# Kernel tuning notes

Hardware: AMD Instinct MI355X
Metric: run time of the kernel (lower is better)

## Reference

```python
import jax, jax.numpy as jnp
import numpy as np

B, T, M, P = 512, 64, 256, 256


def setup_inputs() -> dict:
    key = jax.random.key(0)
    ks = jax.random.split(key, 17)
    w = lambda i, shape: (jax.random.normal(ks[i], shape, jnp.float32) * 0.05)
    return {
        "encoded_inputs": jax.random.normal(ks[0], (B, T, M), jnp.float32),
        "y": jax.random.normal(ks[1], (B, T, 1), jnp.float32),
        "tar": jax.random.normal(ks[2], (B, 2), jnp.float32),
        "train": 1,
        "Wd_w": w(3, (M, 2 * P)), "Wd_b": w(4, (M,)),
        "Ud_w": w(5, (M, M)),
        "vd_w": w(6, (1, M)),
        "wt_w": w(7, (1, M + 1)), "wt_b": w(8, (1,)),
        "Wy_w": w(9, (P, P + M)), "Wy_b": w(10, (P,)),
        "vy_w": w(11, (1, P)), "vy_b": w(12, (1,)),
        "Wih": w(13, (4 * P, 1)), "Whh": w(14, (4 * P, P)),
        "bih": w(15, (4 * P,)), "bhh": w(16, (4 * P,)),
    }


def _lstm_cell(x, h, c, Wih, Whh, bih, bhh):
    # torch.nn.LSTMCell gate order: i, f, g, o
    g = x @ Wih.T + h @ Whh.T + (bih + bhh)
    i, f, gg, o = jnp.split(g, 4, axis=1)
    c = jax.nn.sigmoid(f) * c + jax.nn.sigmoid(i) * jnp.tanh(gg)
    h = jax.nn.sigmoid(o) * jnp.tanh(c)
    return h, c


def reference(encoded_inputs, y, tar, train,
              Wd_w, Wd_b, Ud_w, vd_w, wt_w, wt_b,
              Wy_w, Wy_b, vy_w, vy_b, Wih, Whh, bih, bhh):
    Bn = encoded_inputs.shape[0]
    Pn = Whh.shape[1]
    Mn = encoded_inputs.shape[2]
    h0 = jnp.zeros((Bn, Pn), encoded_inputs.dtype)
    c0 = jnp.zeros((Bn, Pn), encoded_inputs.dtype)
    ctx0 = jnp.zeros((Bn, Mn), encoded_inputs.dtype)
    # U_d(encoded_inputs) is loop-invariant
    y1 = jnp.einsum('btm,nm->btn', encoded_inputs, Ud_w)  # (B,T,M)

    def attend(h, s):
        x1 = jnp.concatenate([h, s], axis=1) @ Wd_w.T + Wd_b      # (B,M)
        z1 = jnp.tanh(x1[:, None, :] + y1)                        # (B,T,M)
        l = jnp.einsum('btm,m->bt', z1, vd_w[0])                  # (B,T)
        beta = jax.nn.softmax(l, axis=1)
        return jnp.einsum('bt,btm->bm', beta, encoded_inputs)     # (B,M)

    def step(carry, y_t):
        h, s, _ = carry
        c_t = attend(h, s)
        y_til = jnp.concatenate([c_t, y_t], axis=1) @ wt_w.T + wt_b  # (B,1)
        h, s = _lstm_cell(y_til, h, s, Wih, Whh, bih, bhh)
        return (h, s, c_t), None

    (h, s, c_t), _ = jax.lax.scan(step, (h0, c0, ctx0), jnp.swapaxes(y, 0, 1))

    def head(h):
        return (jnp.concatenate([h, c_t], axis=1) @ Wy_w.T + Wy_b) @ vy_w.T + vy_b

    def extra(h, s, inp):
        y_til = jnp.concatenate([c_t, inp], axis=1) @ wt_w.T + wt_b
        h, s = _lstm_cell(y_til, h, s, Wih, Whh, bih, bhh)
        return h, s, head(h)

    y_Tp1 = head(h)
    if train:
        h, s, y_Tp2 = extra(h, s, tar[:, 0:1])
        h, s, y_Tp3 = extra(h, s, tar[:, 1:2])
    else:
        h, s, y_Tp2 = extra(h, s, y_Tp1)
        h, s, y_Tp3 = extra(h, s, y_Tp2)
    return (y_Tp1, y_Tp2, y_Tp3)
```

## Files before the change

kernel.cpp:

```cpp
#include <hip/hip_runtime.h>


typedef unsigned short u16;
typedef unsigned int u32;
typedef _Float16 half_t;
typedef half_t h2 __attribute__((ext_vector_type(2)));

#define BB 512
#define TT 64
#define MM 256
#define PP 256
#define YS 264
#define ES 68

#define WD16_OFF  0
#define WHH16_OFF 131072
#define WY16_OFF  393216
#define WQ_ELEMS  524288
#define WQ_BYTES  (WQ_ELEMS * 2)

struct H8 { h2 p[4]; };

#if defined(__has_builtin)
#if __has_builtin(__builtin_amdgcn_fdot2)
#define FDOT2(a, b, c) __builtin_amdgcn_fdot2((a), (b), (c), false)
#endif
#endif
#ifndef FDOT2
__device__ __forceinline__ float FDOT2(h2 a, h2 b, float c) {
  return c + (float)a[0] * (float)b[0] + (float)a[1] * (float)b[1];
}
#endif

__device__ __forceinline__ float dot8(const H8 w, const H8 a, float acc) {
  acc = FDOT2(w.p[0], a.p[0], acc);
  acc = FDOT2(w.p[1], a.p[1], acc);
  acc = FDOT2(w.p[2], a.p[2], acc);
  acc = FDOT2(w.p[3], a.p[3], acc);
  return acc;
}
__device__ __forceinline__ u16 f2h(float f) {
  union { half_t h; u16 u; } x; x.h = (half_t)f; return x.u;
}
__device__ __forceinline__ void unpackH8(const H8 v, float f[8]) {
#pragma unroll
  for (int i = 0; i < 8; ++i) f[i] = (float)v.p[i >> 1][i & 1];
}
__device__ __forceinline__ void ldf8(const float* p, float f[8]) {
  float4 a = *(const float4*)p;
  float4 b = *(const float4*)(p + 4);
  f[0]=a.x; f[1]=a.y; f[2]=a.z; f[3]=a.w;
  f[4]=b.x; f[5]=b.y; f[6]=b.z; f[7]=b.w;
}
__device__ __forceinline__ float tanh_fast(float x) {
  float e = __builtin_amdgcn_exp2f(x * 2.885390081777927f);
  return 1.0f - 2.0f * __builtin_amdgcn_rcpf(1.0f + e);
}
__device__ __forceinline__ float sigmoid_fast(float x) {
  float e = __builtin_amdgcn_exp2f(x * -1.4426950408889634f);
  return __builtin_amdgcn_rcpf(1.0f + e);
}

__global__ __launch_bounds__(256) void prep_kernel(
    const float* __restrict__ Wd, const float* __restrict__ Whh,
    const float* __restrict__ Wy, u16* __restrict__ o) {
  int i = blockIdx.x * 256 + threadIdx.x;
  float v;
  if (i < WHH16_OFF) {
    int ki = i & 7, n = (i >> 3) & 255, kb = i >> 11;
    v = Wd[n * 512 + kb * 8 + ki];
  } else if (i < WY16_OFF) {
    int r = i - WHH16_OFF;
    int ki = r & 7, n = (r >> 3) & 1023, kb = r >> 13;
    v = Whh[n * 256 + kb * 8 + ki];
  } else {
    int r = i - WY16_OFF;
    int ki = r & 7, n = (r >> 3) & 255, kb = r >> 11;
    v = Wy[n * 512 + kb * 8 + ki];
  }
  o[i] = f2h(v);
}

template <int WQ>
__global__ __launch_bounds__(256, 2) void scan_kernel(
    const float* __restrict__ E,
    const float* __restrict__ yin,
    const float* __restrict__ tar,
    const int*   __restrict__ train,
    const void*  __restrict__ Wd_q,
    const float* __restrict__ Wd_b,
    const float* __restrict__ Ud_w,
    const float* __restrict__ vd_w,
    const float* __restrict__ wt_w,
    const float* __restrict__ wt_b,
    const void*  __restrict__ Wy_q,
    const float* __restrict__ Wy_b,
    const float* __restrict__ vy_w,
    const float* __restrict__ vy_b,
    const float* __restrict__ Wih,
    const void*  __restrict__ Whh_q,
    const float* __restrict__ bih,
    const float* __restrict__ bhh,
    float* __restrict__ out)
{
  __shared__ __align__(16) u16   y1l[TT * YS];
  __shared__ __align__(16) u16   e16T[MM * ES];
  __shared__ __align__(16) u32   hs16[256];
  __shared__ __align__(16) u32   ctx16p[128];
  __shared__ __align__(16) float ctx[MM];
  __shared__ __align__(16) float x1s[MM];
  __shared__ __align__(16) float lpart[4][TT];
  __shared__ __align__(16) u16   betas16[TT];
  __shared__ float red[4];
  __shared__ float sc[2];

  const int j = threadIdx.x;
  const int b = blockIdx.x;
  const int wv = j >> 6;

  hs16[j] = 0;
  float creg = 0.f;

  {
    const float* __restrict__ Eb = E + (size_t)b * TT * MM;
    for (int i = j; i < TT * MM; i += 256) {
      int t = i >> 8, m = i & 255;
      e16T[m * ES + t] = f2h(Eb[i]);
    }
  }

  {
    const float* __restrict__ Eb = E + (size_t)b * TT * MM;
    const float* __restrict__ Uj = Ud_w + (size_t)j * MM;
    for (int t0 = 0; t0 < TT; t0 += 16) {
      float acc[16];
#pragma unroll
      for (int i = 0; i < 16; ++i) acc[i] = 0.f;
      for (int m0 = 0; m0 < MM; m0 += 8) {
        float w[8]; ldf8(Uj + m0, w);
#pragma unroll
        for (int tt = 0; tt < 16; ++tt) {
          float e[8]; ldf8(Eb + (size_t)(t0 + tt) * MM + m0, e);
#pragma unroll
          for (int mm = 0; mm < 8; ++mm) acc[tt] = fmaf(e[mm], w[mm], acc[tt]);
        }
      }
#pragma unroll
      for (int tt = 0; tt < 16; ++tt)
        y1l[(t0 + tt) * YS + j] = f2h(acc[tt]);
    }
  }
  __syncthreads();

  auto mv4 = [&](float& g0, float& g1, float& g2, float& g3) {
    g0 = g1 = g2 = g3 = 0.f;
    if (WQ) {
      const u16* W = (const u16*)Whh_q;
      const u16* p0 = W + (size_t)j * 8;
      const u16* p1 = p0 + 256 * 8;
      const u16* p2 = p0 + 512 * 8;
      const u16* p3 = p0 + 768 * 8;
#pragma unroll 4
      for (int kb = 0; kb < 32; ++kb) {
        H8 hp = *(const H8*)&hs16[kb * 4];
        g0 = dot8(*(const H8*)p0, hp, g0); p0 += 8192;
        g1 = dot8(*(const H8*)p1, hp, g1); p1 += 8192;
        g2 = dot8(*(const H8*)p2, hp, g2); p2 += 8192;
        g3 = dot8(*(const H8*)p3, hp, g3); p3 += 8192;
      }
    } else {
      const float* W = (const float*)Whh_q;
      const float* p0 = W + (size_t)j * 256;
#pragma unroll 2
      for (int kb = 0; kb < 32; ++kb) {
        H8 hp = *(const H8*)&hs16[kb * 4];
        float hf[8]; unpackH8(hp, hf);
        float w0[8], w1[8], w2[8], w3[8];
        ldf8(p0 + kb * 8, w0);
        ldf8(p0 + 256 * 256 + kb * 8, w1);
        ldf8(p0 + 512 * 256 + kb * 8, w2);
        ldf8(p0 + 768 * 256 + kb * 8, w3);
#pragma unroll
        for (int i = 0; i < 8; ++i) {
          g0 = fmaf(hf[i], w0[i], g0);
          g1 = fmaf(hf[i], w1[i], g1);
          g2 = fmaf(hf[i], w2[i], g2);
          g3 = fmaf(hf[i], w3[i], g3);
        }
      }
    }
  };

  auto gates_apply = [&](float g0, float g1, float g2, float g3, float ytil) {
    g0 += ytil * Wih[j]       + bih[j]       + bhh[j];
    g1 += ytil * Wih[j + 256] + bih[j + 256] + bhh[j + 256];
    g2 += ytil * Wih[j + 512] + bih[j + 512] + bhh[j + 512];
    g3 += ytil * Wih[j + 768] + bih[j + 768] + bhh[j + 768];
    float c = sigmoid_fast(g1) * creg + sigmoid_fast(g0) * tanh_fast(g2);
    float h = sigmoid_fast(g3) * tanh_fast(c);
    creg = c;
    u16* hsu = (u16*)hs16;
    hsu[j] = f2h(h);
    hsu[256 + j] = f2h(c);
  };

  auto head_store = [&](int outIdx) {
    float p = 0.f;
    if (WQ) {
      const u16* W = (const u16*)Wy_q;
      const u16* ph = W + (size_t)j * 8;
      const u16* pc = W + (size_t)(32 * 256 + j) * 8;
#pragma unroll 4
      for (int kb = 0; kb < 32; ++kb) {
        H8 hp = *(const H8*)&hs16[kb * 4];
        H8 cp = *(const H8*)&ctx16p[kb * 4];
        p = dot8(*(const H8*)ph, hp, p); ph += 2048;
        p = dot8(*(const H8*)pc, cp, p); pc += 2048;
      }
    } else {
      const float* W = (const float*)Wy_q + (size_t)j * 512;
      for (int kb = 0; kb < 32; ++kb) {
        H8 hp = *(const H8*)&hs16[kb * 4];
        float hf[8]; unpackH8(hp, hf);
        float w0[8], w1[8];
        ldf8(W + kb * 8, w0);
        ldf8(W + 256 + kb * 8, w1);
#pragma unroll
        for (int i = 0; i < 8; ++i) {
          p = fmaf(hf[i], w0[i], p);
          p = fmaf(ctx[kb * 8 + i], w1[i], p);
        }
      }
    }
    float pp = (p + Wy_b[j]) * vy_w[j];
#pragma unroll
    for (int off = 32; off; off >>= 1) pp += __shfl_xor(pp, off, 64);
    if ((j & 63) == 0) red[wv] = pp;
    __syncthreads();
    if (j == 0) {
      float o = red[0] + red[1] + red[2] + red[3] + vy_b[0];
      out[(size_t)outIdx * BB + b] = o;
      sc[0] = o;
    }
    __syncthreads();
  };

  for (int step = 0; step < TT; ++step) {
    float ax0 = 0.f, ax1 = 0.f, g0, g1, g2, g3;
    {
      if (WQ) {
        const u16* Wd16 = (const u16*)Wd_q;
        const u16* Wh16 = (const u16*)Whh_q;
        const u16* pdh = Wd16 + (size_t)j * 8;
        const u16* pdc = Wd16 + (size_t)(32 * 256 + j) * 8;
        const u16* p0 = Wh16 + (size_t)j * 8;
        const u16* p1 = p0 + 256 * 8;
        const u16* p2 = p0 + 512 * 8;
        const u16* p3 = p0 + 768 * 8;
        float b0 = 0.f, b1 = 0.f, b2 = 0.f, b3 = 0.f;
#pragma unroll 4
        for (int kb = 0; kb < 32; ++kb) {
          H8 hp = *(const H8*)&hs16[kb * 4];
          H8 cp = *(const H8*)&hs16[128 + kb * 4];
          ax0 = dot8(*(const H8*)pdh, hp, ax0); pdh += 2048;
          ax1 = dot8(*(const H8*)pdc, cp, ax1); pdc += 2048;
          b0 = dot8(*(const H8*)p0, hp, b0); p0 += 8192;
          b1 = dot8(*(const H8*)p1, hp, b1); p1 += 8192;
          b2 = dot8(*(const H8*)p2, hp, b2); p2 += 8192;
          b3 = dot8(*(const H8*)p3, hp, b3); p3 += 8192;
        }
        g0 = b0; g1 = b1; g2 = b2; g3 = b3;
      } else {
        const float* wd = (const float*)Wd_q + (size_t)j * 512;
        const float* w0p = (const float*)Whh_q + (size_t)j * 256;
        float b0 = 0.f, b1 = 0.f, b2 = 0.f, b3 = 0.f;
#pragma unroll 2
        for (int kb = 0; kb < 32; ++kb) {
          H8 hp = *(const H8*)&hs16[kb * 4];
          H8 cp = *(const H8*)&hs16[128 + kb * 4];
          float hf[8], cf[8]; unpackH8(hp, hf); unpackH8(cp, cf);
          float wh[8], wc[8], w0[8], w1[8], w2[8], w3[8];
          ldf8(wd + kb * 8, wh);
          ldf8(wd + 256 + kb * 8, wc);
          ldf8(w0p + kb * 8, w0);
          ldf8(w0p + 256 * 256 + kb * 8, w1);
          ldf8(w0p + 512 * 256 + kb * 8, w2);
          ldf8(w0p + 768 * 256 + kb * 8, w3);
#pragma unroll
          for (int i = 0; i < 8; ++i) {
            ax0 = fmaf(hf[i], wh[i], ax0);
            ax1 = fmaf(cf[i], wc[i], ax1);
            b0 = fmaf(hf[i], w0[i], b0);
            b1 = fmaf(hf[i], w1[i], b1);
            b2 = fmaf(hf[i], w2[i], b2);
            b3 = fmaf(hf[i], w3[i], b3);
          }
        }
        g0 = b0; g1 = b1; g2 = b2; g3 = b3;
      }
      x1s[j] = ax0 + ax1 + Wd_b[j];
    }
    __syncthreads();

    {
      const int q = wv, tq = j & 63;
      const u16* __restrict__ yrow = &y1l[tq * YS + q * 64];
      const float* __restrict__ xp = &x1s[q * 64];
      const float* __restrict__ vp = vd_w + q * 64;
      float lp = 0.f;
#pragma unroll 2
      for (int m0 = 0; m0 < 64; m0 += 8) {
        H8 yv = *(const H8*)(yrow + m0);
        float yf[8]; unpackH8(yv, yf);
        float xf[8]; ldf8(xp + m0, xf);
        float vf[8]; ldf8(vp + m0, vf);
#pragma unroll
        for (int mm = 0; mm < 8; ++mm) {
          float z = tanh_fast(xf[mm] + yf[mm]);
          lp = fmaf(z, vf[mm], lp);
        }
      }
      lpart[q][tq] = lp;
    }
    __syncthreads();

    if (j < 64) {
      const int t = j;
      float l = lpart[0][t] + lpart[1][t] + lpart[2][t] + lpart[3][t];
      float mx = l;
#pragma unroll
      for (int off = 32; off; off >>= 1) mx = fmaxf(mx, __shfl_xor(mx, off, 64));
      float e = __builtin_amdgcn_exp2f((l - mx) * 1.4426950408889634f);
      float sm = e;
#pragma unroll
      for (int off = 32; off; off >>= 1) sm += __shfl_xor(sm, off, 64);
      betas16[t] = f2h(e * __builtin_amdgcn_rcpf(sm));
    }
    __syncthreads();

    {
      const u16* __restrict__ ep = &e16T[j * ES];
      float acc = 0.f;
#pragma unroll
      for (int t0 = 0; t0 < TT; t0 += 8) {
        h2 e0 = *(const h2*)(ep + t0);
        h2 e1 = *(const h2*)(ep + t0 + 2);
        h2 e2 = *(const h2*)(ep + t0 + 4);
        h2 e3 = *(const h2*)(ep + t0 + 6);
        H8 bp = *(const H8*)&betas16[t0];
        acc = FDOT2(bp.p[0], e0, acc);
        acc = FDOT2(bp.p[1], e1, acc);
        acc = FDOT2(bp.p[2], e2, acc);
        acc = FDOT2(bp.p[3], e3, acc);
      }
      ctx[j] = acc;
      ((u16*)ctx16p)[j] = f2h(acc);
    }
    {
      float p = ctx[j] * wt_w[j];
#pragma unroll
      for (int off = 32; off; off >>= 1) p += __shfl_xor(p, off, 64);
      if ((j & 63) == 0) red[wv] = p;
    }
    __syncthreads();
    {
      float ytil = red[0] + red[1] + red[2] + red[3]
                 + yin[(size_t)b * TT + step] * wt_w[MM] + wt_b[0];
      gates_apply(g0, g1, g2, g3, ytil);
    }
    __syncthreads();
  }

  float ctdot;
  {
    float p = ctx[j] * wt_w[j];
#pragma unroll
    for (int off = 32; off; off >>= 1) p += __shfl_xor(p, off, 64);
    if ((j & 63) == 0) red[wv] = p;
    __syncthreads();
    ctdot = red[0] + red[1] + red[2] + red[3];
    __syncthreads();
  }

  head_store(0);

  const int tr = train[0];
  for (int e = 0; e < 2; ++e) {
    float inp = tr ? tar[(size_t)b * 2 + e] : sc[0];
    float ytil = ctdot + inp * wt_w[MM] + wt_b[0];
    float g0, g1, g2, g3;
    mv4(g0, g1, g2, g3);
    gates_apply(g0, g1, g2, g3, ytil);
    __syncthreads();
    head_store(1 + e);
  }
}

extern "C" void kernel_launch(void* const* d_in, const int* in_sizes, int n_in,
                              void* d_out, int out_size, void* d_ws, size_t ws_size,
                              hipStream_t stream) {
  const float* E     = (const float*)d_in[0];
  const float* yin   = (const float*)d_in[1];
  const float* tar   = (const float*)d_in[2];
  const int*   train = (const int*)d_in[3];
  const float* Wd_w  = (const float*)d_in[4];
  const float* Wd_b  = (const float*)d_in[5];
  const float* Ud_w  = (const float*)d_in[6];
  const float* vd_w  = (const float*)d_in[7];
  const float* wt_w  = (const float*)d_in[8];
  const float* wt_b  = (const float*)d_in[9];
  const float* Wy_w  = (const float*)d_in[10];
  const float* Wy_b  = (const float*)d_in[11];
  const float* vy_w  = (const float*)d_in[12];
  const float* vy_b  = (const float*)d_in[13];
  const float* Wih   = (const float*)d_in[14];
  const float* Whh   = (const float*)d_in[15];
  const float* bih   = (const float*)d_in[16];
  const float* bhh   = (const float*)d_in[17];

  float* out = (float*)d_out;

  if (ws_size >= (size_t)WQ_BYTES) {
    u16* wq = (u16*)d_ws;
    prep_kernel<<<dim3(WQ_ELEMS / 256), dim3(256), 0, stream>>>(
        Wd_w, Whh, Wy_w, wq);
    scan_kernel<1><<<dim3(BB), dim3(256), 0, stream>>>(
        E, yin, tar, train, wq + WD16_OFF, Wd_b, Ud_w, vd_w, wt_w, wt_b,
        wq + WY16_OFF, Wy_b, vy_w, vy_b, Wih, wq + WHH16_OFF, bih, bhh, out);
  } else {
    scan_kernel<0><<<dim3(BB), dim3(256), 0, stream>>>(
        E, yin, tar, train, Wd_w, Wd_b, Ud_w, vd_w, wt_w, wt_b,
        Wy_w, Wy_b, vy_w, vy_b, Wih, Whh, bih, bhh, out);
  }

  (void)in_sizes; (void)n_in; (void)out_size;
}
```

Baseline: 1.192 ms.

## Fold context dot into precomputed E·wt and split work over 512 threads

Precomputes E·wt per timestep so the per-step context's wt projection reduces to a softmax-weighted sum of scalars, removing the per-step context vector computation and the fp16 transposed E copy in LDS. Context is only materialised once after the loop for the head. Block size doubles to 512 threads, with the Wd and Wy matvecs split across halves and Whh gates written through shared memory, and loop-invariant LSTM biases hoisted into registers. This trades lower occupancy and extra LDS traffic and syncs for less redundant per-step work.

```diff
diff --git a/kernel.cpp b/kernel.cpp
--- a/kernel.cpp
+++ b/kernel.cpp
@@ -9,9 +9,8 @@
 #define BB 512
 #define TT 64
 #define MM 256
-#define PP 256
 #define YS 264
-#define ES 68
+#define NTH 512
 
 #define WD16_OFF  0
 #define WHH16_OFF 131072
@@ -82,7 +81,7 @@
 }
 
 template <int WQ>
-__global__ __launch_bounds__(256, 2) void scan_kernel(
+__global__ __launch_bounds__(NTH) void scan_kernel(
     const float* __restrict__ E,
     const float* __restrict__ yin,
     const float* __restrict__ tar,
@@ -104,35 +103,52 @@
     float* __restrict__ out)
 {
   __shared__ __align__(16) u16   y1l[TT * YS];
-  __shared__ __align__(16) u16   e16T[MM * ES];
   __shared__ __align__(16) u32   hs16[256];
   __shared__ __align__(16) u32   ctx16p[128];
-  __shared__ __align__(16) float ctx[MM];
-  __shared__ __align__(16) float x1s[MM];
-  __shared__ __align__(16) float lpart[4][TT];
-  __shared__ __align__(16) u16   betas16[TT];
-  __shared__ float red[4];
-  __shared__ float sc[2];
-
-  const int j = threadIdx.x;
-  const int b = blockIdx.x;
-  const int wv = j >> 6;
-
-  hs16[j] = 0;
+  __shared__ __align__(16) float px1[2][MM];
+  __shared__ __align__(16) float gg[1024];
+  __shared__ __align__(16) float lpart[8][TT];
+  __shared__ __align__(16) float bet[TT];
+  __shared__ __align__(16) float ysh[TT];
+  __shared__ __align__(16) float ewl[TT];
+  __shared__ float red[8];
+  __shared__ float sc[1];
+
+  const int j    = threadIdx.x;
+  const int n    = j & 255;
+  const int half = j >> 8;
+  const int wv   = j >> 6;
+  const int b    = blockIdx.x;
+
+  if (j < 256) hs16[j] = 0;
   float creg = 0.f;
+
+  const float wih0 = Wih[n],       wih1 = Wih[n + 256];
+  const float wih2 = Wih[n + 512], wih3 = Wih[n + 768];
+  const float bb0 = bih[n]       + bhh[n];
+  const float bb1 = bih[n + 256] + bhh[n + 256];
+  const float bb2 = bih[n + 512] + bhh[n + 512];
+  const float bb3 = bih[n + 768] + bhh[n + 768];
+  const float wtM = wt_w[MM], wtb = wt_b[0];
+
+  if (j < TT) {
+    const int t = j;
+    ysh[t] = yin[(size_t)b * TT + t];
+    const float* __restrict__ Er = E + ((size_t)b * TT + t) * MM;
+    float acc = 0.f;
+    for (int m0 = 0; m0 < MM; m0 += 8) {
+      float e[8], w[8];
+      ldf8(Er + m0, e); ldf8(wt_w + m0, w);
+#pragma unroll
+      for (int m = 0; m < 8; ++m) acc = fmaf(e[m], w[m], acc);
+    }
+    ewl[t] = acc;
+  }
 
   {
     const float* __restrict__ Eb = E + (size_t)b * TT * MM;
-    for (int i = j; i < TT * MM; i += 256) {
-      int t = i >> 8, m = i & 255;
-      e16T[m * ES + t] = f2h(Eb[i]);
-    }
-  }
-
-  {
-    const float* __restrict__ Eb = E + (size_t)b * TT * MM;
-    const float* __restrict__ Uj = Ud_w + (size_t)j * MM;
-    for (int t0 = 0; t0 < TT; t0 += 16) {
+    const float* __restrict__ Uj = Ud_w + (size_t)n * MM;
+    for (int t0 = half * 32; t0 < half * 32 + 32; t0 += 16) {
       float acc[16];
 #pragma unroll
       for (int i = 0; i < 16; ++i) acc[i] = 0.f;
@@ -147,95 +163,92 @@
       }
 #pragma unroll
       for (int tt = 0; tt < 16; ++tt)
-        y1l[(t0 + tt) * YS + j] = f2h(acc[tt]);
+        y1l[(t0 + tt) * YS + n] = f2h(acc[tt]);
     }
   }
   __syncthreads();
 
-  auto mv4 = [&](float& g0, float& g1, float& g2, float& g3) {
-    g0 = g1 = g2 = g3 = 0.f;
+  auto gates_apply = [&](float gi, float gf, float gG, float go, float ytil) {
+    gi += ytil * wih0 + bb0;
+    gf += ytil * wih1 + bb1;
+    gG += ytil * wih2 + bb2;
+    go += ytil * wih3 + bb3;
+    float c = sigmoid_fast(gf) * creg + sigmoid_fast(gi) * tanh_fast(gG);
+    float h = sigmoid_fast(go) * tanh_fast(c);
+    creg = c;
+    u16* hsu = (u16*)hs16;
+    hsu[n] = f2h(h);
+    hsu[256 + n] = f2h(c);
+  };
+
+  auto whh_gg = [&]() {
+    float g1 = 0.f, g2 = 0.f;
     if (WQ) {
-      const u16* W = (const u16*)Whh_q;
-      const u16* p0 = W + (size_t)j * 8;
-      const u16* p1 = p0 + 256 * 8;
-      const u16* p2 = p0 + 512 * 8;
-      const u16* p3 = p0 + 768 * 8;
+      const u16* __restrict__ pw = (const u16*)Whh_q + (size_t)j * 8;
 #pragma unroll 4
       for (int kb = 0; kb < 32; ++kb) {
-        H8 hp = *(const H8*)&hs16[kb * 4];
-        g0 = dot8(*(const H8*)p0, hp, g0); p0 += 8192;
-        g1 = dot8(*(const H8*)p1, hp, g1); p1 += 8192;
-        g2 = dot8(*(const H8*)p2, hp, g2); p2 += 8192;
-        g3 = dot8(*(const H8*)p3, hp, g3); p3 += 8192;
+        H8 w1 = *(const H8*)pw;
+        H8 w2 = *(const H8*)(pw + 4096);
+        pw += 8192;
+        H8 hv = *(const H8*)&hs16[kb * 4];
+        g1 = dot8(w1, hv, g1);
+        g2 = dot8(w2, hv, g2);
       }
     } else {
-      const float* W = (const float*)Whh_q;
-      const float* p0 = W + (size_t)j * 256;
+      const float* __restrict__ p1 = (const float*)Whh_q + (size_t)j * 256;
+      const float* __restrict__ p2 = (const float*)Whh_q +
+                                     ((size_t)j + 512) * 256;
 #pragma unroll 2
       for (int kb = 0; kb < 32; ++kb) {
-        H8 hp = *(const H8*)&hs16[kb * 4];
-        float hf[8]; unpackH8(hp, hf);
-        float w0[8], w1[8], w2[8], w3[8];
-        ldf8(p0 + kb * 8, w0);
-        ldf8(p0 + 256 * 256 + kb * 8, w1);
-        ldf8(p0 + 512 * 256 + kb * 8, w2);
-        ldf8(p0 + 768 * 256 + kb * 8, w3);
-#pragma unroll
-        for (int i = 0; i < 8; ++i) {
-          g0 = fmaf(hf[i], w0[i], g0);
-          g1 = fmaf(hf[i], w1[i], g1);
-          g2 = fmaf(hf[i], w2[i], g2);
-          g3 = fmaf(hf[i], w3[i], g3);
+        H8 hv = *(const H8*)&hs16[kb * 4];
+        float hf[8]; unpackH8(hv, hf);
+        float w1[8], w2[8];
+        ldf8(p1 + kb * 8, w1); ldf8(p2 + kb * 8, w2);
+#pragma unroll
+        for (int m = 0; m < 8; ++m) {
+          g1 = fmaf(hf[m], w1[m], g1);
+          g2 = fmaf(hf[m], w2[m], g2);
         }
       }
     }
+    gg[j] = g1;
+    gg[j + 512] = g2;
   };
 
-  auto gates_apply = [&](float g0, float g1, float g2, float g3, float ytil) {
-    g0 += ytil * Wih[j]       + bih[j]       + bhh[j];
-    g1 += ytil * Wih[j + 256] + bih[j + 256] + bhh[j + 256];
-    g2 += ytil * Wih[j + 512] + bih[j + 512] + bhh[j + 512];
-    g3 += ytil * Wih[j + 768] + bih[j + 768] + bhh[j + 768];
-    float c = sigmoid_fast(g1) * creg + sigmoid_fast(g0) * tanh_fast(g2);
-    float h = sigmoid_fast(g3) * tanh_fast(c);
-    creg = c;
-    u16* hsu = (u16*)hs16;
-    hsu[j] = f2h(h);
-    hsu[256 + j] = f2h(c);
+  auto gates_from_gg = [&](float ytil) {
+    gates_apply(gg[n], gg[n + 256], gg[n + 512], gg[n + 768], ytil);
   };
 
   auto head_store = [&](int outIdx) {
     float p = 0.f;
+    const u32* st = half ? ctx16p : hs16;
     if (WQ) {
-      const u16* W = (const u16*)Wy_q;
-      const u16* ph = W + (size_t)j * 8;
-      const u16* pc = W + (size_t)(32 * 256 + j) * 8;
-#pragma unroll 4
+      const u16* pw = (const u16*)Wy_q + ((size_t)(half * 32) * 256 + n) * 8;
+#pragma unroll 2
       for (int kb = 0; kb < 32; ++kb) {
-        H8 hp = *(const H8*)&hs16[kb * 4];
-        H8 cp = *(const H8*)&ctx16p[kb * 4];
-        p = dot8(*(const H8*)ph, hp, p); ph += 2048;
-        p = dot8(*(const H8*)pc, cp, p); pc += 2048;
+        H8 w = *(const H8*)pw; pw += 2048;
+        H8 s = *(const H8*)&st[kb * 4];
+        p = dot8(w, s, p);
       }
     } else {
-      const float* W = (const float*)Wy_q + (size_t)j * 512;
+      const float* W = (const float*)Wy_q + (size_t)n * 512 + half * 256;
+#pragma unroll 2
       for (int kb = 0; kb < 32; ++kb) {
-        H8 hp = *(const H8*)&hs16[kb * 4];
-        float hf[8]; unpackH8(hp, hf);
-        float w0[8], w1[8];
-        ldf8(W + kb * 8, w0);
-        ldf8(W + 256 + kb * 8, w1);
-#pragma unroll
-        for (int i = 0; i < 8; ++i) {
-          p = fmaf(hf[i], w0[i], p);
-          p = fmaf(ctx[kb * 8 + i], w1[i], p);
-        }
-      }
-    }
-    float pp = (p + Wy_b[j]) * vy_w[j];
-#pragma unroll
-    for (int off = 32; off; off >>= 1) pp += __shfl_xor(pp, off, 64);
-    if ((j & 63) == 0) red[wv] = pp;
+        H8 sv = *(const H8*)&st[kb * 4];
+        float sf[8]; unpackH8(sv, sf);
+        float w[8]; ldf8(W + kb * 8, w);
+#pragma unroll
+        for (int i = 0; i < 8; ++i) p = fmaf(sf[i], w[i], p);
+      }
+    }
+    px1[half][n] = p;
+    __syncthreads();
+    if (j < 256) {
+      float q = (px1[0][n] + px1[1][n] + Wy_b[n]) * vy_w[n];
+#pragma unroll
+      for (int off = 32; off; off >>= 1) q += __shfl_xor(q, off, 64);
+      if ((j & 63) == 0) red[wv] = q;
+    }
     __syncthreads();
     if (j == 0) {
       float o = red[0] + red[1] + red[2] + red[3] + vy_b[0];
@@ -246,151 +259,118 @@
   };
 
   for (int step = 0; step < TT; ++step) {
-    float ax0 = 0.f, ax1 = 0.f, g0, g1, g2, g3;
     {
+      float ax = 0.f;
       if (WQ) {
-        const u16* Wd16 = (const u16*)Wd_q;
-        const u16* Wh16 = (const u16*)Whh_q;
-        const u16* pdh = Wd16 + (size_t)j * 8;
-        const u16* pdc = Wd16 + (size_t)(32 * 256 + j) * 8;
-        const u16* p0 = Wh16 + (size_t)j * 8;
-        const u16* p1 = p0 + 256 * 8;
-        const u16* p2 = p0 + 512 * 8;
-        const u16* p3 = p0 + 768 * 8;
-        float b0 = 0.f, b1 = 0.f, b2 = 0.f, b3 = 0.f;
+        const u16* pd = (const u16*)Wd_q + ((size_t)(half * 32) * 256 + n) * 8;
 #pragma unroll 4
-        for (int kb = 0; kb < 32; ++kb) {
-          H8 hp = *(const H8*)&hs16[kb * 4];
-          H8 cp = *(const H8*)&hs16[128 + kb * 4];
-          ax0 = dot8(*(const H8*)pdh, hp, ax0); pdh += 2048;
-          ax1 = dot8(*(const H8*)pdc, cp, ax1); pdc += 2048;
-          b0 = dot8(*(const H8*)p0, hp, b0); p0 += 8192;
-          b1 = dot8(*(const H8*)p1, hp, b1); p1 += 8192;
-          b2 = dot8(*(const H8*)p2, hp, b2); p2 += 8192;
-          b3 = dot8(*(const H8*)p3, hp, b3); p3 += 8192;
+        for (int i = 0; i < 32; ++i) {
+          H8 w = *(const H8*)pd; pd += 2048;
+          H8 s = *(const H8*)&hs16[(half * 32 + i) * 4];
+          ax = dot8(w, s, ax);
         }
-        g0 = b0; g1 = b1; g2 = b2; g3 = b3;
       } else {
-        const float* wd = (const float*)Wd_q + (size_t)j * 512;
-        const float* w0p = (const float*)Whh_q + (size_t)j * 256;
-        float b0 = 0.f, b1 = 0.f, b2 = 0.f, b3 = 0.f;
+        const float* pd = (const float*)Wd_q + (size_t)n * 512 + half * 256;
 #pragma unroll 2
-        for (int kb = 0; kb < 32; ++kb) {
-          H8 hp = *(const H8*)&hs16[kb * 4];
-          H8 cp = *(const H8*)&hs16[128 + kb * 4];
-          float hf[8], cf[8]; unpackH8(hp, hf); unpackH8(cp, cf);
-          float wh[8], wc[8], w0[8], w1[8], w2[8], w3[8];
-          ldf8(wd + kb * 8, wh);
-          ldf8(wd + 256 + kb * 8, wc);
-          ldf8(w0p + kb * 8, w0);
-          ldf8(w0p + 256 * 256 + kb * 8, w1);
-          ldf8(w0p + 512 * 256 + kb * 8, w2);
-          ldf8(w0p + 768 * 256 + kb * 8, w3);
-#pragma unroll
-          for (int i = 0; i < 8; ++i) {
-            ax0 = fmaf(hf[i], wh[i], ax0);
-            ax1 = fmaf(cf[i], wc[i], ax1);
-            b0 = fmaf(hf[i], w0[i], b0);
-            b1 = fmaf(hf[i], w1[i], b1);
-            b2 = fmaf(hf[i], w2[i], b2);
-            b3 = fmaf(hf[i], w3[i], b3);
-          }
+        for (int i = 0; i < 32; ++i) {
+          H8 sv = *(const H8*)&hs16[(half * 32 + i) * 4];
+          float sf[8]; unpackH8(sv, sf);
+          float w[8]; ldf8(pd + i * 8, w);
+#pragma unroll
+          for (int m = 0; m < 8; ++m) ax = fmaf(sf[m], w[m], ax);
         }
-        g0 = b0; g1 = b1; g2 = b2; g3 = b3;
-      }
-      x1s[j] = ax0 + ax1 + Wd_b[j];
+      }
+      if (half == 0) ax += Wd_b[n];
+      px1[half][n] = ax;
+      whh_gg();
     }
     __syncthreads();
 
     {
-      const int q = wv, tq = j & 63;
-      const u16* __restrict__ yrow = &y1l[tq * YS + q * 64];
-      const float* __restrict__ xp = &x1s[q * 64];
-      const float* __restrict__ vp = vd_w + q * 64;
+      const int t = j & 63;
+      const int mb = wv * 32;
+      const u16* __restrict__ yrow = &y1l[t * YS + mb];
+      const float* __restrict__ xh = &px1[0][mb];
+      const float* __restrict__ xc = &px1[1][mb];
+      const float* __restrict__ vp = vd_w + mb;
       float lp = 0.f;
-#pragma unroll 2
-      for (int m0 = 0; m0 < 64; m0 += 8) {
+#pragma unroll
+      for (int m0 = 0; m0 < 32; m0 += 8) {
         H8 yv = *(const H8*)(yrow + m0);
         float yf[8]; unpackH8(yv, yf);
-        float xf[8]; ldf8(xp + m0, xf);
+        float xf[8]; ldf8(xh + m0, xf);
+        float xg[8]; ldf8(xc + m0, xg);
         float vf[8]; ldf8(vp + m0, vf);
 #pragma unroll
         for (int mm = 0; mm < 8; ++mm) {
-          float z = tanh_fast(xf[mm] + yf[mm]);
+          float z = tanh_fast(xf[mm] + xg[mm] + yf[mm]);
           lp = fmaf(z, vf[mm], lp);
         }
       }
-      lpart[q][tq] = lp;
-    }
-    __syncthreads();
-
-    if (j < 64) {
-      const int t = j;
-      float l = lpart[0][t] + lpart[1][t] + lpart[2][t] + lpart[3][t];
+      lpart[wv][t] = lp;
+    }
+    __syncthreads();
+
+    if (j < 256) {
+      const int t = j & 63;
+      float l = lpart[0][t] + lpart[1][t] + lpart[2][t] + lpart[3][t] +
+                lpart[4][t] + lpart[5][t] + lpart[6][t] + lpart[7][t];
       float mx = l;
 #pragma unroll
       for (int off = 32; off; off >>= 1) mx = fmaxf(mx, __shfl_xor(mx, off, 64));
       float e = __builtin_amdgcn_exp2f((l - mx) * 1.4426950408889634f);
-      float sm = e;
-#pragma unroll
-      for (int off = 32; off; off >>= 1) sm += __shfl_xor(sm, off, 64);
-      betas16[t] = f2h(e * __builtin_amdgcn_rcpf(sm));
-    }
-    __syncthreads();
-
-    {
-      const u16* __restrict__ ep = &e16T[j * ES];
-      float acc = 0.f;
-#pragma unroll
-      for (int t0 = 0; t0 < TT; t0 += 8) {
-        h2 e0 = *(const h2*)(ep + t0);
-        h2 e1 = *(const h2*)(ep + t0 + 2);
-        h2 e2 = *(const h2*)(ep + t0 + 4);
-        h2 e3 = *(const h2*)(ep + t0 + 6);
-        H8 bp = *(const H8*)&betas16[t0];
-        acc = FDOT2(bp.p[0], e0, acc);
-        acc = FDOT2(bp.p[1], e1, acc);
-        acc = FDOT2(bp.p[2], e2, acc);
-        acc = FDOT2(bp.p[3], e3, acc);
-      }
-      ctx[j] = acc;
-      ((u16*)ctx16p)[j] = f2h(acc);
-    }
-    {
-      float p = ctx[j] * wt_w[j];
-#pragma unroll
-      for (int off = 32; off; off >>= 1) p += __shfl_xor(p, off, 64);
-      if ((j & 63) == 0) red[wv] = p;
-    }
-    __syncthreads();
-    {
-      float ytil = red[0] + red[1] + red[2] + red[3]
-                 + yin[(size_t)b * TT + step] * wt_w[MM] + wt_b[0];
-      gates_apply(g0, g1, g2, g3, ytil);
-    }
-    __syncthreads();
-  }
-
-  float ctdot;
-  {
-    float p = ctx[j] * wt_w[j];
+      float se = e, sy = e * ewl[t];
+#pragma unroll
+      for (int off = 32; off; off >>= 1) {
+        se += __shfl_xor(se, off, 64);
+        sy += __shfl_xor(sy, off, 64);
+      }
+      float yt = sy * __builtin_amdgcn_rcpf(se) + ysh[step] * wtM + wtb;
+      gates_from_gg(yt);
+    }
+    __syncthreads();
+  }
+
+  if (j < TT) {
+    const int t = j;
+    float l = lpart[0][t] + lpart[1][t] + lpart[2][t] + lpart[3][t] +
+              lpart[4][t] + lpart[5][t] + lpart[6][t] + lpart[7][t];
+    float mx = l;
+#pragma unroll
+    for (int off = 32; off; off >>= 1) mx = fmaxf(mx, __shfl_xor(mx, off, 64));
+    float e = __builtin_amdgcn_exp2f((l - mx) * 1.4426950408889634f);
+    float sm = e;
+#pragma unroll
+    for (int off = 32; off; off >>= 1) sm += __shfl_xor(sm, off, 64);
+    bet[t] = e * __builtin_amdgcn_rcpf(sm);
+  }
+  __syncthreads();
+
+  if (j < 256) {
+    const float* __restrict__ Eb = E + (size_t)b * TT * MM + n;
+    float acc = 0.f;
+#pragma unroll 8
+    for (int t = 0; t < TT; ++t) acc = fmaf(bet[t], Eb[(size_t)t * MM], acc);
+    ((u16*)ctx16p)[n] = f2h(acc);
+    float p = acc * wt_w[n];
 #pragma unroll
     for (int off = 32; off; off >>= 1) p += __shfl_xor(p, off, 64);
     if ((j & 63) == 0) red[wv] = p;
-    __syncthreads();
-    ctdot = red[0] + red[1] + red[2] + red[3];
-    __syncthreads();
-  }
+  }
+  __syncthreads();
+  const float ctd = red[0] + red[1] + red[2] + red[3];
 
   head_store(0);
 
   const int tr = train[0];
   for (int e = 0; e < 2; ++e) {
-    float inp = tr ? tar[(size_t)b * 2 + e] : sc[0];
-    float ytil = ctdot + inp * wt_w[MM] + wt_b[0];
-    float g0, g1, g2, g3;
-    mv4(g0, g1, g2, g3);
-    gates_apply(g0, g1, g2, g3, ytil);
+    whh_gg();
+    __syncthreads();
+    if (j < 256) {
+      float inp = tr ? tar[(size_t)b * 2 + e] : sc[0];
+      float yt = ctd + inp * wtM + wtb;
+      gates_from_gg(yt);
+    }
     __syncthreads();
     head_store(1 + e);
   }
@@ -424,11 +404,11 @@
     u16* wq = (u16*)d_ws;
     prep_kernel<<<dim3(WQ_ELEMS / 256), dim3(256), 0, stream>>>(
         Wd_w, Whh, Wy_w, wq);
-    scan_kernel<1><<<dim3(BB), dim3(256), 0, stream>>>(
+    scan_kernel<1><<<dim3(BB), dim3(NTH), 0, stream>>>(
         E, yin, tar, train, wq + WD16_OFF, Wd_b, Ud_w, vd_w, wt_w, wt_b,
         wq + WY16_OFF, Wy_b, vy_w, vy_b, Wih, wq + WHH16_OFF, bih, bhh, out);
   } else {
-    scan_kernel<0><<<dim3(BB), dim3(256), 0, stream>>>(
+    scan_kernel<0><<<dim3(BB), dim3(NTH), 0, stream>>>(
         E, yin, tar, train, Wd_w, Wd_b, Ud_w, vd_w, wt_w, wt_b,
         Wy_w, Wy_b, vy_w, vy_b, Wih, Whh, bih, bhh, out);
   }
```

Result: slower. 1.292 ms (+8.3%).
